# Performance work log

Measured on AMD Instinct MI355X. Metric: run time of the kernel, lower is better.

The kernel has to match this reference:

```python
import jax, jax.numpy as jnp
import numpy as np

N_NODES = 100000
N_EDGES = 640000
D = 128
BN_EPS = 1e-5


def setup_inputs() -> dict:
    key = jax.random.key(0)
    ks = jax.random.split(key, 8)
    scale = 1.0 / np.sqrt(D)
    x = jax.random.normal(ks[0], (N_NODES, D), jnp.float32)
    edge_index = jax.random.randint(ks[1], (2, N_EDGES), 0, N_NODES, jnp.int32)
    edge_attr = jax.random.normal(ks[2], (N_EDGES,), jnp.float32)
    # SAGEConv params: lin_l applied to aggregated neighbors (has bias), lin_r to root
    W_l = jax.random.normal(ks[3], (D, D), jnp.float32) * scale
    b_l = jnp.zeros((D,), jnp.float32)
    W_r = jax.random.normal(ks[4], (D, D), jnp.float32) * scale
    # BatchNorm1d affine params
    gamma = jnp.ones((D,), jnp.float32)
    beta = jnp.zeros((D,), jnp.float32)
    return {"x": x, "edge_attr": edge_attr, "W_l": W_l, "b_l": b_l,
            "W_r": W_r, "gamma": gamma, "beta": beta, "edge_index": edge_index}


def reference(x, edge_attr, W_l, b_l, W_r, gamma, beta, edge_index):
    n = x.shape[0]
    h = jax.nn.relu(x)                               # ReLU before conv
    src, dst = edge_index[0], edge_index[1]
    msg = h[src]                                     # gather [E, D]
    agg = jax.ops.segment_sum(msg, dst, num_segments=n)          # scatter-add [N, D]
    cnt = jax.ops.segment_sum(jnp.ones((msg.shape[0], 1), h.dtype), dst,
                              num_segments=n)
    mean_agg = agg / jnp.maximum(cnt, 1.0)           # mean aggregation (clamp deg>=1)
    out = mean_agg @ W_l.T + b_l + h @ W_r.T         # SAGEConv: neighbor + root terms
    # BatchNorm1d (training mode: batch stats, biased variance)
    mu = jnp.mean(out, axis=0)
    var = jnp.mean(jnp.square(out - mu), axis=0)
    xhat = (out - mu) * jax.lax.rsqrt(var + BN_EPS)
    return xhat * gamma + beta
```

## Files before the change

kernel.cpp:

```cpp
#include <hip/hip_runtime.h>
#include <stdint.h>

#define NN 100000
#define NE 640000
#define DD 128
#define BN_EPS 1e-5f
#define NB 391
#define NROWPAD 100096
#define NTILE 782
#define GGRID 512

typedef __attribute__((ext_vector_type(8)))  short bf16x8;
typedef __attribute__((ext_vector_type(4)))  float f32x4;

static __device__ __forceinline__ float bf2f(unsigned short s) {
  return __uint_as_float(((unsigned)s) << 16);
}
static __device__ __forceinline__ unsigned short f2bf(float f) {
  unsigned u = __float_as_uint(f);
  u += 0x7FFFu + ((u >> 16) & 1u);
  return (unsigned short)(u >> 16);
}

__global__ __launch_bounds__(1024) void k_zero(int* __restrict__ deg)
{
  int i = blockIdx.x * 1024 + threadIdx.x;
  if (i < NROWPAD) deg[i] = 0;
}

__global__ __launch_bounds__(256) void k_setup(
    const float* __restrict__ x,
    const float* __restrict__ Wl, const float* __restrict__ Wr,
    const int* __restrict__ ei,
    unsigned short* __restrict__ abuf, unsigned short* __restrict__ wbf,
    int* __restrict__ deg)
{
  int b = blockIdx.x;
  if ((b & 3) == 3) {
    int e = (b >> 2) * 256 + threadIdx.x;
    if (e < NE) atomicAdd(deg + ei[NE + e], 1);
    return;
  }
  int rank = b - (b >> 2);
  if (rank < 6256) {
    int i = rank * 256 + threadIdx.x;
    int row = i >> 4, cj = i & 15;
    if (row < NN) {
      const float* xp = x + (long)row * DD + cj * 8;
      float tmp[8];
      *(float4*)(tmp)     = *(const float4*)(xp);
      *(float4*)(tmp + 4) = *(const float4*)(xp + 4);
      bf16x8 o;
#pragma unroll
      for (int e = 0; e < 8; ++e) o[e] = (short)f2bf(fmaxf(tmp[e], 0.f));
      *(bf16x8*)(abuf + (long)row * 256 + DD + cj * 8) = o;
    } else {
      bf16x8 z = {};
      *(bf16x8*)(abuf + (long)row * 256 + cj * 8) = z;
      *(bf16x8*)(abuf + (long)row * 256 + DD + cj * 8) = z;
    }
  } else if (rank < 6384) {
    int i = (rank - 6256) * 256 + threadIdx.x;
    int col = i >> 8, k = i & 255;
    float v = (k < DD) ? Wl[col * DD + k] : Wr[col * DD + (k - DD)];
    wbf[i] = f2bf(v);
  }
}

__global__ __launch_bounds__(256) void k_scan1(const int* __restrict__ deg,
                                               int* __restrict__ bsum)
{
  __shared__ int sc[256];
  int t = threadIdx.x;
  sc[t] = deg[blockIdx.x * 256 + t];
  __syncthreads();
  for (int s = 128; s > 0; s >>= 1) {
    if (t < s) sc[t] += sc[t + s];
    __syncthreads();
  }
  if (t == 0) bsum[blockIdx.x] = sc[0];
}

__global__ __launch_bounds__(256) void k_scan3(int* __restrict__ deg,
                                               const int* __restrict__ bsum,
                                               int* __restrict__ offs)
{
  __shared__ int sc[256];
  __shared__ int pre[256];
  int t = threadIdx.x;
  int p = 0;
  for (int j = t; j < blockIdx.x; j += 256) p += bsum[j];
  pre[t] = p;
  __syncthreads();
  for (int s = 128; s > 0; s >>= 1) {
    if (t < s) pre[t] += pre[t + s];
    __syncthreads();
  }
  int boff = pre[0];
  __syncthreads();
  int i = blockIdx.x * 256 + t;
  int v = deg[i];
  sc[t] = v;
  __syncthreads();
  for (int s = 1; s < 256; s <<= 1) {
    int add = (t >= s) ? sc[t - s] : 0;
    __syncthreads();
    sc[t] += add;
    __syncthreads();
  }
  int excl = sc[t] - v + boff;
  offs[i] = excl;
  deg[i]  = excl;
}

__global__ __launch_bounds__(256) void k_fill(const int* __restrict__ ei,
                                              int* __restrict__ cursor,
                                              int* __restrict__ esrc)
{
  int e = blockIdx.x * 256 + threadIdx.x;
  if (e >= NE) return;
  int pos = atomicAdd(cursor + ei[NE + e], 1);
  esrc[pos] = ei[e];
}

__global__ __launch_bounds__(256) void k_agg(const int* __restrict__ offs,
                                             const int* __restrict__ esrc,
                                             unsigned short* __restrict__ abuf)
{
  int dst = blockIdx.x * 4 + (threadIdx.x >> 6);
  if (dst >= NN) return;
  int lane = threadIdx.x & 63;
  int q  = lane >> 4;
  int fl = lane & 15;
  int off = offs[dst], end = offs[dst + 1];
  int deg = end - off;
  float acc[8];
#pragma unroll
  for (int e = 0; e < 8; ++e) acc[e] = 0.f;

  for (int base = off; base < end; base += 64) {
    int m = end - base; if (m > 64) m = 64;
    int mysrc = (base + lane < end) ? esrc[base + lane] : NN;
    int iters = (m + 3) >> 2;
#pragma unroll 2
    for (int i = 0; i < iters; ++i) {
      int src = __shfl(mysrc, i * 4 + q);
      bf16x8 w = *(const bf16x8*)(abuf + (long)src * 256 + DD + fl * 8);
#pragma unroll
      for (int e = 0; e < 8; ++e) acc[e] += bf2f((unsigned short)w[e]);
    }
  }

#pragma unroll
  for (int e = 0; e < 8; ++e) {
    acc[e] += __shfl_xor(acc[e], 16);
    acc[e] += __shfl_xor(acc[e], 32);
  }
  if (q == 0) {
    float rinv = (deg > 0) ? 1.0f / (float)deg : 0.f;
    bf16x8 o;
#pragma unroll
    for (int e = 0; e < 8; ++e) o[e] = (short)f2bf(acc[e] * rinv);
    *(bf16x8*)(abuf + (long)dst * 256 + fl * 8) = o;
  }
}

#define GEMM_STAGE_B() \
  _Pragma("unroll") \
  for (int j = 0; j < 8; ++j) { \
    int id = j * 512 + t, col = id >> 5, seg = id & 31; \
    uint4 v = *(const uint4*)(wbf + col * 256 + seg * 8); \
    int byte = (col << 9) + (seg << 4); byte ^= (col & 7) << 4; \
    *(uint4*)((char*)blds + byte) = v; \
  } \
  __syncthreads();

#define GEMM_TILE_COMPUTE(rb) \
  { const unsigned short* ap = abuf + (long)((rb) + c15) * 256 + kg * 8; \
    _Pragma("unroll 4") \
    for (int ks = 0; ks < 8; ++ks) { \
      bf16x8 a = *(const bf16x8*)(ap + ks * 32); \
      _Pragma("unroll") \
      for (int ct = 0; ct < 8; ++ct) { \
        int byte = ((ct * 16 + c15) << 9) + (ks << 6) + (kg << 4); \
        byte ^= (c15 & 7) << 4; \
        bf16x8 b = *(const bf16x8*)((const char*)blds + byte); \
        acc[ct] = __builtin_amdgcn_mfma_f32_16x16x32_bf16(a, b, acc[ct], 0, 0, 0); \
      } \
    } }

__global__ __launch_bounds__(512, 2) void k_gemm1(
    unsigned short* __restrict__ abuf,
    const unsigned short* __restrict__ wbf,
    float* __restrict__ partials)
{
  __shared__ __align__(16) unsigned short blds[32768];
  const int t = threadIdx.x;
  const int lane = t & 63, wv = t >> 6;
  const int c15 = lane & 15, kg = lane >> 4;

  GEMM_STAGE_B();

  float sS[8], sQ[8];
#pragma unroll
  for (int ct = 0; ct < 8; ++ct) { sS[ct] = 0.f; sQ[ct] = 0.f; }

  for (int tile = blockIdx.x; tile < NTILE; tile += GGRID) {
    int rb = tile * 128 + wv * 16;
    f32x4 acc[8];
#pragma unroll
    for (int ct = 0; ct < 8; ++ct) acc[ct] = (f32x4){0.f, 0.f, 0.f, 0.f};
    GEMM_TILE_COMPUTE(rb);
#pragma unroll
    for (int ct = 0; ct < 8; ++ct) {
      int col = ct * 16 + c15;
#pragma unroll
      for (int r = 0; r < 4; ++r) {
        float v = acc[ct][r];
        sS[ct] += v;
        sQ[ct] += v * v;
        abuf[(long)(rb + kg * 4 + r) * 256 + col] = f2bf(v);
      }
    }
  }

  __syncthreads();
  float* slds = (float*)blds;
#pragma unroll
  for (int ct = 0; ct < 8; ++ct) {
    float s = sS[ct], q = sQ[ct];
    s += __shfl_xor(s, 16); q += __shfl_xor(q, 16);
    s += __shfl_xor(s, 32); q += __shfl_xor(q, 32);
    if (lane < 16) {
      slds[wv * 256 + ct * 16 + lane] = s;
      slds[wv * 256 + 128 + ct * 16 + lane] = q;
    }
  }
  __syncthreads();
  if (t < 256) {
    float a = 0.f;
#pragma unroll
    for (int w = 0; w < 8; ++w) a += slds[w * 256 + t];
    partials[blockIdx.x * 256 + t] = a;
  }
}

__global__ __launch_bounds__(1024) void k_stats(
    const float* __restrict__ partials, const float* __restrict__ bl,
    const float* __restrict__ gamma, const float* __restrict__ beta,
    float* __restrict__ ss)
{
  __shared__ float red[4][256];
  int t = threadIdx.x & 255, g = threadIdx.x >> 8;
  float a = 0.f;
#pragma unroll 8
  for (int blk = g; blk < GGRID; blk += 4) a += partials[blk * 256 + t];
  red[g][t] = a;
  __syncthreads();
  if (threadIdx.x < 256)
    red[0][t] = red[0][t] + red[1][t] + red[2][t] + red[3][t];
  __syncthreads();
  if (threadIdx.x < 128) {
    float Sr = red[0][t], Qr = red[0][128 + t];
    float b  = bl[t];
    float S  = Sr + (float)NN * b;
    float Q  = Qr + 2.f * b * Sr + (float)NN * b * b;
    float mu  = S / (float)NN;
    float var = Q / (float)NN - mu * mu;
    float rsig = rsqrtf(var + BN_EPS);
    float sc  = gamma[t] * rsig;
    float sh2 = beta[t] - mu * sc;
    ss[t]       = sc;
    ss[128 + t] = b * sc + sh2;
  }
}

__global__ __launch_bounds__(256) void k_norm(
    const unsigned short* __restrict__ abuf,
    const float* __restrict__ ss,
    float* __restrict__ out)
{
  __shared__ float sc[128], sh[128];
  if (threadIdx.x < 128) {
    sc[threadIdx.x] = ss[threadIdx.x];
    sh[threadIdx.x] = ss[128 + threadIdx.x];
  }
  __syncthreads();
  int i = blockIdx.x * 256 + threadIdx.x;
  int row = i >> 4, cj = i & 15;
  if (row >= NN) return;
  bf16x8 v = *(const bf16x8*)(abuf + (long)row * 256 + cj * 8);
  int c0 = cj * 8;
  float4 o0, o1;
  o0.x = fmaf(bf2f((unsigned short)v[0]), sc[c0 + 0], sh[c0 + 0]);
  o0.y = fmaf(bf2f((unsigned short)v[1]), sc[c0 + 1], sh[c0 + 1]);
  o0.z = fmaf(bf2f((unsigned short)v[2]), sc[c0 + 2], sh[c0 + 2]);
  o0.w = fmaf(bf2f((unsigned short)v[3]), sc[c0 + 3], sh[c0 + 3]);
  o1.x = fmaf(bf2f((unsigned short)v[4]), sc[c0 + 4], sh[c0 + 4]);
  o1.y = fmaf(bf2f((unsigned short)v[5]), sc[c0 + 5], sh[c0 + 5]);
  o1.z = fmaf(bf2f((unsigned short)v[6]), sc[c0 + 6], sh[c0 + 6]);
  o1.w = fmaf(bf2f((unsigned short)v[7]), sc[c0 + 7], sh[c0 + 7]);
  *(float4*)(out + (long)row * DD + c0)     = o0;
  *(float4*)(out + (long)row * DD + c0 + 4) = o1;
}

extern "C" void kernel_launch(void* const* d_in, const int* in_sizes, int n_in,
                              void* d_out, int out_size, void* d_ws, size_t ws_size,
                              hipStream_t stream)
{
  const float* x     = (const float*)d_in[0];
  const float* Wl    = (const float*)d_in[2];
  const float* bl    = (const float*)d_in[3];
  const float* Wr    = (const float*)d_in[4];
  const float* gamma = (const float*)d_in[5];
  const float* beta  = (const float*)d_in[6];
  const int*   ei    = (const int*)d_in[7];
  float* out = (float*)d_out;

  char* ws = (char*)d_ws;
  unsigned short* abuf = (unsigned short*)(ws);
  int*   esrc  = (int*)(ws + 51249152);
  int*   deg   = (int*)(ws + 53809152);
  int*   offs  = (int*)(ws + 54209536);
  int*   bsum  = (int*)(ws + 54609920);
  unsigned short* wbf = (unsigned short*)(ws + 54611968);
  float* partials = (float*)esrc;
  float* ssbuf    = (float*)deg;
  (void)ws_size; (void)in_sizes; (void)n_in; (void)out_size;

  k_zero  <<<98,   1024, 0, stream>>>(deg);
  k_setup <<<10000, 256, 0, stream>>>(x, Wl, Wr, ei, abuf, wbf, deg);
  k_scan1 <<<NB,    256, 0, stream>>>(deg, bsum);
  k_scan3 <<<NB,    256, 0, stream>>>(deg, bsum, offs);
  k_fill  <<<2500,  256, 0, stream>>>(ei, deg, esrc);
  k_agg   <<<25000, 256, 0, stream>>>(offs, esrc, abuf);
  k_gemm1 <<<GGRID, 512, 0, stream>>>(abuf, wbf, partials);
  k_stats <<<1,    1024, 0, stream>>>(partials, bl, gamma, beta, ssbuf);
  k_norm  <<<6250,  256, 0, stream>>>(abuf, ssbuf, out);
}
```

Measured before the change: 154.4 us.

## Split interleaved activation buffer into separate compact x and aggregate arrays

The single 256-wide bf16 buffer holding [mean_agg | relu(x)] per row is replaced by two separate 128-wide arrays. The neighbour gather in aggregation now reads from a dense array, which may improve cache-line locality, and the GEMM loads its A operand from two pointers. The GEMM output is written compactly into the aggregate array. The normalization kernel is also changed to a persistent grid-stride loop over tiles with 512-thread blocks, in the same tile order the GEMM used, likely to reuse data still in cache.

```diff
diff --git a/kernel.cpp b/kernel.cpp
--- a/kernel.cpp
+++ b/kernel.cpp
@@ -22,6 +22,7 @@
   return (unsigned short)(u >> 16);
 }
 
+
 __global__ __launch_bounds__(1024) void k_zero(int* __restrict__ deg)
 {
   int i = blockIdx.x * 1024 + threadIdx.x;
@@ -32,8 +33,8 @@
     const float* __restrict__ x,
     const float* __restrict__ Wl, const float* __restrict__ Wr,
     const int* __restrict__ ei,
-    unsigned short* __restrict__ abuf, unsigned short* __restrict__ wbf,
-    int* __restrict__ deg)
+    unsigned short* __restrict__ xbf, unsigned short* __restrict__ magg,
+    unsigned short* __restrict__ wbf, int* __restrict__ deg)
 {
   int b = blockIdx.x;
   if ((b & 3) == 3) {
@@ -53,11 +54,11 @@
       bf16x8 o;
 #pragma unroll
       for (int e = 0; e < 8; ++e) o[e] = (short)f2bf(fmaxf(tmp[e], 0.f));
-      *(bf16x8*)(abuf + (long)row * 256 + DD + cj * 8) = o;
+      *(bf16x8*)(xbf + (long)row * DD + cj * 8) = o;
     } else {
       bf16x8 z = {};
-      *(bf16x8*)(abuf + (long)row * 256 + cj * 8) = z;
-      *(bf16x8*)(abuf + (long)row * 256 + DD + cj * 8) = z;
+      *(bf16x8*)(xbf  + (long)row * DD + cj * 8) = z;
+      *(bf16x8*)(magg + (long)row * DD + cj * 8) = z;
     }
   } else if (rank < 6384) {
     int i = (rank - 6256) * 256 + threadIdx.x;
@@ -125,7 +126,8 @@
 
 __global__ __launch_bounds__(256) void k_agg(const int* __restrict__ offs,
                                              const int* __restrict__ esrc,
-                                             unsigned short* __restrict__ abuf)
+                                             const unsigned short* __restrict__ xbf,
+                                             unsigned short* __restrict__ magg)
 {
   int dst = blockIdx.x * 4 + (threadIdx.x >> 6);
   if (dst >= NN) return;
@@ -145,7 +147,7 @@
 #pragma unroll 2
     for (int i = 0; i < iters; ++i) {
       int src = __shfl(mysrc, i * 4 + q);
-      bf16x8 w = *(const bf16x8*)(abuf + (long)src * 256 + DD + fl * 8);
+      bf16x8 w = *(const bf16x8*)(xbf + (long)src * DD + fl * 8);
 #pragma unroll
       for (int e = 0; e < 8; ++e) acc[e] += bf2f((unsigned short)w[e]);
     }
@@ -161,7 +163,7 @@
     bf16x8 o;
 #pragma unroll
     for (int e = 0; e < 8; ++e) o[e] = (short)f2bf(acc[e] * rinv);
-    *(bf16x8*)(abuf + (long)dst * 256 + fl * 8) = o;
+    *(bf16x8*)(magg + (long)dst * DD + fl * 8) = o;
   }
 }
 
@@ -176,10 +178,12 @@
   __syncthreads();
 
 #define GEMM_TILE_COMPUTE(rb) \
-  { const unsigned short* ap = abuf + (long)((rb) + c15) * 256 + kg * 8; \
+  { const unsigned short* ap0 = magg + (long)((rb) + c15) * DD + kg * 8; \
+    const unsigned short* ap1 = xbf  + (long)((rb) + c15) * DD + kg * 8; \
     _Pragma("unroll 4") \
     for (int ks = 0; ks < 8; ++ks) { \
-      bf16x8 a = *(const bf16x8*)(ap + ks * 32); \
+      bf16x8 a = (ks < 4) ? *(const bf16x8*)(ap0 + ks * 32) \
+                          : *(const bf16x8*)(ap1 + (ks - 4) * 32); \
       _Pragma("unroll") \
       for (int ct = 0; ct < 8; ++ct) { \
         int byte = ((ct * 16 + c15) << 9) + (ks << 6) + (kg << 4); \
@@ -190,7 +194,8 @@
     } }
 
 __global__ __launch_bounds__(512, 2) void k_gemm1(
-    unsigned short* __restrict__ abuf,
+    unsigned short* __restrict__ magg,
+    const unsigned short* __restrict__ xbf,
     const unsigned short* __restrict__ wbf,
     float* __restrict__ partials)
 {
@@ -219,7 +224,7 @@
         float v = acc[ct][r];
         sS[ct] += v;
         sQ[ct] += v * v;
-        abuf[(long)(rb + kg * 4 + r) * 256 + col] = f2bf(v);
+        magg[(long)(rb + kg * 4 + r) * DD + col] = f2bf(v);
       }
     }
   }
@@ -275,8 +280,8 @@
   }
 }
 
-__global__ __launch_bounds__(256) void k_norm(
-    const unsigned short* __restrict__ abuf,
+__global__ __launch_bounds__(512) void k_norm(
+    const unsigned short* __restrict__ magg,
     const float* __restrict__ ss,
     float* __restrict__ out)
 {
@@ -286,22 +291,26 @@
     sh[threadIdx.x] = ss[128 + threadIdx.x];
   }
   __syncthreads();
-  int i = blockIdx.x * 256 + threadIdx.x;
-  int row = i >> 4, cj = i & 15;
-  if (row >= NN) return;
-  bf16x8 v = *(const bf16x8*)(abuf + (long)row * 256 + cj * 8);
-  int c0 = cj * 8;
-  float4 o0, o1;
-  o0.x = fmaf(bf2f((unsigned short)v[0]), sc[c0 + 0], sh[c0 + 0]);
-  o0.y = fmaf(bf2f((unsigned short)v[1]), sc[c0 + 1], sh[c0 + 1]);
-  o0.z = fmaf(bf2f((unsigned short)v[2]), sc[c0 + 2], sh[c0 + 2]);
-  o0.w = fmaf(bf2f((unsigned short)v[3]), sc[c0 + 3], sh[c0 + 3]);
-  o1.x = fmaf(bf2f((unsigned short)v[4]), sc[c0 + 4], sh[c0 + 4]);
-  o1.y = fmaf(bf2f((unsigned short)v[5]), sc[c0 + 5], sh[c0 + 5]);
-  o1.z = fmaf(bf2f((unsigned short)v[6]), sc[c0 + 6], sh[c0 + 6]);
-  o1.w = fmaf(bf2f((unsigned short)v[7]), sc[c0 + 7], sh[c0 + 7]);
-  *(float4*)(out + (long)row * DD + c0)     = o0;
-  *(float4*)(out + (long)row * DD + c0 + 4) = o1;
+  for (int tile = blockIdx.x; tile < NTILE; tile += GGRID) {
+    long tb = (long)tile * 128;
+    for (int i = threadIdx.x; i < 2048; i += 512) {
+      long row = tb + (i >> 4);
+      if (row >= NN) continue;
+      int c0 = (i & 15) * 8;
+      bf16x8 v = *(const bf16x8*)(magg + row * DD + c0);
+      float4 o0, o1;
+      o0.x = fmaf(bf2f((unsigned short)v[0]), sc[c0 + 0], sh[c0 + 0]);
+      o0.y = fmaf(bf2f((unsigned short)v[1]), sc[c0 + 1], sh[c0 + 1]);
+      o0.z = fmaf(bf2f((unsigned short)v[2]), sc[c0 + 2], sh[c0 + 2]);
+      o0.w = fmaf(bf2f((unsigned short)v[3]), sc[c0 + 3], sh[c0 + 3]);
+      o1.x = fmaf(bf2f((unsigned short)v[4]), sc[c0 + 4], sh[c0 + 4]);
+      o1.y = fmaf(bf2f((unsigned short)v[5]), sc[c0 + 5], sh[c0 + 5]);
+      o1.z = fmaf(bf2f((unsigned short)v[6]), sc[c0 + 6], sh[c0 + 6]);
+      o1.w = fmaf(bf2f((unsigned short)v[7]), sc[c0 + 7], sh[c0 + 7]);
+      *(float4*)(out + row * DD + c0)     = o0;
+      *(float4*)(out + row * DD + c0 + 4) = o1;
+    }
+  }
 }
 
 extern "C" void kernel_launch(void* const* d_in, const int* in_sizes, int n_in,
@@ -318,7 +327,8 @@
   float* out = (float*)d_out;
 
   char* ws = (char*)d_ws;
-  unsigned short* abuf = (unsigned short*)(ws);
+  unsigned short* magg = (unsigned short*)(ws);
+  unsigned short* xbf  = (unsigned short*)(ws + 25624576);
   int*   esrc  = (int*)(ws + 51249152);
   int*   deg   = (int*)(ws + 53809152);
   int*   offs  = (int*)(ws + 54209536);
@@ -329,12 +339,12 @@
   (void)ws_size; (void)in_sizes; (void)n_in; (void)out_size;
 
   k_zero  <<<98,   1024, 0, stream>>>(deg);
-  k_setup <<<10000, 256, 0, stream>>>(x, Wl, Wr, ei, abuf, wbf, deg);
+  k_setup <<<10000, 256, 0, stream>>>(x, Wl, Wr, ei, xbf, magg, wbf, deg);
   k_scan1 <<<NB,    256, 0, stream>>>(deg, bsum);
   k_scan3 <<<NB,    256, 0, stream>>>(deg, bsum, offs);
   k_fill  <<<2500,  256, 0, stream>>>(ei, deg, esrc);
-  k_agg   <<<25000, 256, 0, stream>>>(offs, esrc, abuf);
-  k_gemm1 <<<GGRID, 512, 0, stream>>>(abuf, wbf, partials);
+  k_agg   <<<25000, 256, 0, stream>>>(offs, esrc, xbf, magg);
+  k_gemm1 <<<GGRID, 512, 0, stream>>>(magg, xbf, wbf, partials);
   k_stats <<<1,    1024, 0, stream>>>(partials, bl, gamma, beta, ssbuf);
-  k_norm  <<<6250,  256, 0, stream>>>(abuf, ssbuf, out);
-}
+  k_norm  <<<GGRID, 512, 0, stream>>>(magg, ssbuf, out);
+}
```

Result: no change. 152.5 us, median of 2 (-1.2%).
